# Optimization experiments

Hardware: AMD Instinct MI355X
Metric: run time of the kernel (lower is better)

Reference implementation:

```python
import jax, jax.numpy as jnp
import numpy as np

B = 262144      # points per batch
DIM = 3         # input_dim
L = 16          # levels
T = 19          # log2 hash table size
F = 2           # features per level
N_MIN, N_MAX = 16, 512

_b = np.exp((np.log(N_MAX) - np.log(N_MIN)) / (L - 1))
RES = np.floor(N_MIN * _b ** np.arange(L)).astype(np.float32).reshape(1, 1, L, 1)

# voxel corner offsets [1, DIM, 1, 2^DIM]
_border = np.empty((DIM, 2 ** DIM), dtype=np.uint32)
for i in range(DIM):
    _border[i, :] = np.array(([0] * 2 ** i + [1] * 2 ** i) * 2 ** (DIM - i - 1), dtype=np.uint32)
BORDER = _border.reshape(1, DIM, 1, 2 ** DIM)

# tiny-cuda-nn hash primes; all fit in uint32. Since the torch code takes the
# result mod 2^T (a power of two), int64 and uint32 arithmetic agree on the
# low bits, so uint32 hashing is bit-exact with the original.
PRIMES = np.array([1, 2654435761, 805459861], dtype=np.uint32)
MASK = np.uint32(2 ** T - 1)


def setup_inputs() -> dict:
    key = jax.random.key(0)
    k1, k2 = jax.random.split(key)
    x = jax.random.uniform(k1, (B, DIM), dtype=jnp.float32)  # coords in [0,1)
    tables = jax.random.uniform(k2, (L, 2 ** T, F), dtype=jnp.float32,
                                minval=-1e-4, maxval=1e-4)
    return {"x": x, "tables": tables}


def reference(x, tables):
    res = jnp.asarray(RES)                                   # [1,1,L,1]
    border = jnp.asarray(BORDER)                             # [1,DIM,1,2^DIM]
    primes = jnp.asarray(PRIMES)
    scaled = x[:, :, None, None] * res                       # [B,DIM,L,1]
    grid = jnp.floor(scaled).astype(jnp.uint32) + border     # [B,DIM,L,2^DIM]
    # spatial hash: xor of per-dim coord * prime, mod 2^T
    h = (grid[:, 0] * primes[0]) ^ (grid[:, 1] * primes[1]) ^ (grid[:, 2] * primes[2])
    idx = (h & MASK).astype(jnp.int32)                       # [B,L,2^DIM]
    gathered = tables[jnp.arange(L)[None, :, None], idx]     # [B,L,2^DIM,F]
    # multilinear interpolation weights
    w = jnp.prod(1.0 - jnp.abs(scaled - grid.astype(scaled.dtype)), axis=1)  # [B,L,2^DIM]
    out = jnp.einsum('blv,blvf->blf', w, gathered)           # [B,L,F]
    return out.reshape(x.shape[0], L * F)
```

## Files before the change

### kernel.cpp

```cpp
#include <hip/hip_runtime.h>


#define NB 262144
#define NL 16
#define TSIZE (1u << 19)
#define TMASK ((1u << 19) - 1u)
#define P1 2654435761u
#define P2 805459861u
#define NBKT 32768

typedef float vf2 __attribute__((ext_vector_type(2)));
typedef float vf4 __attribute__((ext_vector_type(4)));

__constant__ float RES_C[NL] = {16.f, 20.f, 25.f, 32.f, 40.f, 50.f, 64.f, 80.f,
                                101.f, 128.f, 161.f, 203.f, 256.f, 322.f, 406.f, 512.f};

__constant__ int SEQ_C[NL] = {0, 15, 1, 14, 2, 13, 3, 12, 4, 11, 5, 10, 6, 9, 7, 8};

__device__ __forceinline__ int bucket_of(float px, float py, float pz) {
  int bx = min(31, (int)(px * 32.0f));
  int by = min(31, (int)(py * 32.0f));
  int bz = min(31, (int)(pz * 32.0f));
  return bx | (by << 5) | (bz << 10);
}

__device__ __forceinline__ void ngp_point_level(
    float px, float py, float pz, int l, const float* __restrict__ tables,
    float& o0, float& o1) {
  const float res = RES_C[l];
  const float sx = px * res, sy = py * res, sz = pz * res;
  const float fx = floorf(sx), fy = floorf(sy), fz = floorf(sz);
  const unsigned ix = (unsigned)fx, iy = (unsigned)fy, iz = (unsigned)fz;

  const unsigned hx0 = ix, hx1 = ix + 1u;
  const unsigned hy0 = iy * P1, hy1 = hy0 + P1;
  const unsigned hz0 = iz * P2, hz1 = hz0 + P2;

  const float wx0 = 1.0f - fabsf(sx - fx);
  const float wx1 = 1.0f - fabsf(sx - (fx + 1.0f));
  const float wy0 = 1.0f - fabsf(sy - fy);
  const float wy1 = 1.0f - fabsf(sy - (fy + 1.0f));
  const float wz0 = 1.0f - fabsf(sz - fz);
  const float wz1 = 1.0f - fabsf(sz - (fz + 1.0f));

  const vf2* __restrict__ tbl = (const vf2*)tables + (size_t)l * TSIZE;

  unsigned idxs[8];
#pragma unroll
  for (int v = 0; v < 8; ++v) {
    const unsigned hx = (v & 1) ? hx1 : hx0;
    const unsigned hy = (v & 2) ? hy1 : hy0;
    const unsigned hz = (v & 4) ? hz1 : hz0;
    idxs[v] = (hx ^ hy ^ hz) & TMASK;
  }
  vf2 g[8];
#pragma unroll
  for (int v = 0; v < 8; ++v) g[v] = tbl[idxs[v]];

  o0 = 0.0f; o1 = 0.0f;
#pragma unroll
  for (int v = 0; v < 8; ++v) {
    const float w = ((v & 1) ? wx1 : wx0) * ((v & 2) ? wy1 : wy0) * ((v & 4) ? wz1 : wz0);
    o0 = fmaf(w, g[v].x, o0);
    o1 = fmaf(w, g[v].y, o1);
  }
}

__global__ __launch_bounds__(256) void zero_kernel(unsigned* __restrict__ hist) {
  hist[blockIdx.x * 256 + threadIdx.x] = 0u;
}

__global__ __launch_bounds__(256) void hist_kernel(
    const float* __restrict__ x, unsigned* __restrict__ hist) {
  const int b = blockIdx.x * 256 + threadIdx.x;
  const float px = x[b * 3 + 0], py = x[b * 3 + 1], pz = x[b * 3 + 2];
  atomicAdd(&hist[bucket_of(px, py, pz)], 1u);
}

__global__ __launch_bounds__(1024) void scan_kernel(
    const unsigned* __restrict__ hist, unsigned* __restrict__ offs) {
  __shared__ unsigned part[1024];
  const int t = threadIdx.x;
  const int base = t * 32;
  unsigned loc[32];
  unsigned s = 0;
#pragma unroll
  for (int i = 0; i < 32; ++i) { loc[i] = s; s += hist[base + i]; }
  part[t] = s;
  __syncthreads();
  for (int d = 1; d < 1024; d <<= 1) {
    unsigned v = (t >= d) ? part[t - d] : 0u;
    __syncthreads();
    part[t] += v;
    __syncthreads();
  }
  const unsigned pre = (t == 0) ? 0u : part[t - 1];
#pragma unroll
  for (int i = 0; i < 32; ++i) offs[base + i] = pre + loc[i];
}

__global__ __launch_bounds__(256) void scatter_kernel(
    const float* __restrict__ x, unsigned* __restrict__ offs,
    vf4* __restrict__ xp) {
  const int b = blockIdx.x * 256 + threadIdx.x;
  const float px = x[b * 3 + 0], py = x[b * 3 + 1], pz = x[b * 3 + 2];
  const unsigned pos = atomicAdd(&offs[bucket_of(px, py, pz)], 1u);
  vf4 v; v.x = px; v.y = py; v.z = pz; v.w = __uint_as_float((unsigned)b);
  xp[pos] = v;
}

__global__ __launch_bounds__(256) void ngp_gather_sorted_kernel(
    const vf4* __restrict__ xp,
    const float* __restrict__ tables,
    vf2* __restrict__ ws) {
  const int i = blockIdx.x;
  const int lvl = SEQ_C[i >> 10];
  const int chunk = i & 1023;
  const int p = chunk * 256 + threadIdx.x;

  const vf4 v = __builtin_nontemporal_load(xp + p);

  float o0, o1;
  ngp_point_level(v.x, v.y, v.z, lvl, tables, o0, o1);

  vf2 r; r.x = o0; r.y = o1;
  __builtin_nontemporal_store(r, ws + (size_t)lvl * NB + p);
}

__global__ __launch_bounds__(256) void ngp_transpose_sorted_kernel(
    const vf2* __restrict__ ws,
    const vf4* __restrict__ xp,
    vf4* __restrict__ out4) {
  __shared__ vf2 tile[NL][257];
  __shared__ unsigned pid[256];
  const int t = threadIdx.x;
  const int p0 = blockIdx.x * 256;

#pragma unroll
  for (int l = 0; l < NL; ++l) {
    tile[l][t] = __builtin_nontemporal_load(ws + (size_t)l * NB + p0 + t);
  }
  pid[t] = __float_as_uint(xp[p0 + t].w);
  __syncthreads();

#pragma unroll
  for (int k = 0; k < 8; ++k) {
    const int q = k * 256 + t;
    const int pq = q >> 3;
    const int wq = q & 7;
    const vf2 a = tile[2 * wq + 0][pq];
    const vf2 c = tile[2 * wq + 1][pq];
    vf4 v; v.x = a.x; v.y = a.y; v.z = c.x; v.w = c.y;
    out4[(size_t)pid[pq] * 8 + wq] = v;
  }
}

__global__ __launch_bounds__(256) void ngp_gather_kernel(
    const float* __restrict__ x, const float* __restrict__ tables,
    vf2* __restrict__ ws) {
  const int i = blockIdx.x;
  const int lvl = (i & 7) | ((i >> 13) << 3);
  const int chunk = (i >> 3) & 1023;
  const int b = chunk * 256 + threadIdx.x;
  const float px = __builtin_nontemporal_load(x + b * 3 + 0);
  const float py = __builtin_nontemporal_load(x + b * 3 + 1);
  const float pz = __builtin_nontemporal_load(x + b * 3 + 2);
  float o0, o1;
  ngp_point_level(px, py, pz, lvl, tables, o0, o1);
  vf2 r; r.x = o0; r.y = o1;
  __builtin_nontemporal_store(r, ws + (size_t)lvl * NB + b);
}

__global__ __launch_bounds__(256) void ngp_transpose_kernel(
    const vf2* __restrict__ ws, vf4* __restrict__ out4) {
  __shared__ vf2 tile[NL][257];
  const int t = threadIdx.x;
  const int p0 = blockIdx.x * 256;
#pragma unroll
  for (int l = 0; l < NL; ++l) {
    tile[l][t] = __builtin_nontemporal_load(ws + (size_t)l * NB + p0 + t);
  }
  __syncthreads();
#pragma unroll
  for (int k = 0; k < 8; ++k) {
    const int q = k * 256 + t;
    const int pq = q >> 3;
    const int wq = q & 7;
    const vf2 a = tile[2 * wq + 0][pq];
    const vf2 c = tile[2 * wq + 1][pq];
    vf4 v; v.x = a.x; v.y = a.y; v.z = c.x; v.w = c.y;
    __builtin_nontemporal_store(v, out4 + (size_t)p0 * 8 + q);
  }
}

__global__ __launch_bounds__(256) void ngp_fused_kernel(
    const float* __restrict__ x, const float* __restrict__ tables,
    float* __restrict__ out) {
  const int tid = blockIdx.x * blockDim.x + threadIdx.x;
  const int l = tid & (NL - 1);
  const int b = tid >> 4;
  float o0, o1;
  ngp_point_level(x[b * 3], x[b * 3 + 1], x[b * 3 + 2], l, tables, o0, o1);
  float2 r = make_float2(o0, o1);
  ((float2*)out)[tid] = r;
}

extern "C" void kernel_launch(void* const* d_in, const int* in_sizes, int n_in,
                              void* d_out, int out_size, void* d_ws, size_t ws_size,
                              hipStream_t stream) {
  const float* x = (const float*)d_in[0];
  const float* tables = (const float*)d_in[1];
  float* out = (float*)d_out;

  const size_t ws2_b = (size_t)NL * NB * sizeof(vf2);
  const size_t xp_b = (size_t)NB * sizeof(vf4);
  const size_t hist_b = (size_t)NBKT * sizeof(unsigned);
  const size_t sorted_need = ws2_b + xp_b + 2 * hist_b;

  if (ws_size >= sorted_need) {
    char* base = (char*)d_ws;
    vf2* ws2 = (vf2*)base;
    vf4* xp = (vf4*)(base + ws2_b);
    unsigned* hist = (unsigned*)(base + ws2_b + xp_b);
    unsigned* offs = (unsigned*)(base + ws2_b + xp_b + hist_b);

    zero_kernel<<<NBKT / 256, 256, 0, stream>>>(hist);
    hist_kernel<<<NB / 256, 256, 0, stream>>>(x, hist);
    scan_kernel<<<1, 1024, 0, stream>>>(hist, offs);
    scatter_kernel<<<NB / 256, 256, 0, stream>>>(x, offs, xp);
    ngp_gather_sorted_kernel<<<NB * NL / 256, 256, 0, stream>>>(xp, tables, ws2);
    ngp_transpose_sorted_kernel<<<NB / 256, 256, 0, stream>>>(ws2, xp, (vf4*)out);
  } else if (ws_size >= ws2_b) {
    vf2* ws = (vf2*)d_ws;
    ngp_gather_kernel<<<NB * NL / 256, 256, 0, stream>>>(x, tables, ws);
    ngp_transpose_kernel<<<NB / 256, 256, 0, stream>>>(ws, (vf4*)out);
  } else {
    ngp_fused_kernel<<<NB * NL / 256, 256, 0, stream>>>(x, tables, out);
  }
}
```

Measured before the change: 204.7 us.

## Coarsen sort buckets, fuse scan into scatter, gather table pairs as float4

Reduces the spatial sort grid from 32^3 to 16^3 buckets. The separate single-block scan kernel is dropped: every scatter block now recomputes the 4096-entry prefix sum in shared memory and takes ranks from a separate counter array, and the zero kernel becomes a memset. The hash lookup now reads 16-byte aligned pairs of table entries and picks the needed half, aiming for wider loads and fewer launches. The costs are coarser sort locality, a redundant per-block scan, and twice the bytes fetched per corner.

```diff
diff --git a/kernel.cpp b/kernel.cpp
--- a/kernel.cpp
+++ b/kernel.cpp
@@ -7,7 +7,7 @@
 #define TMASK ((1u << 19) - 1u)
 #define P1 2654435761u
 #define P2 805459861u
-#define NBKT 32768
+#define NBKT 4096
 
 typedef float vf2 __attribute__((ext_vector_type(2)));
 typedef float vf4 __attribute__((ext_vector_type(4)));
@@ -18,10 +18,10 @@
 __constant__ int SEQ_C[NL] = {0, 15, 1, 14, 2, 13, 3, 12, 4, 11, 5, 10, 6, 9, 7, 8};
 
 __device__ __forceinline__ int bucket_of(float px, float py, float pz) {
-  int bx = min(31, (int)(px * 32.0f));
-  int by = min(31, (int)(py * 32.0f));
-  int bz = min(31, (int)(pz * 32.0f));
-  return bx | (by << 5) | (bz << 10);
+  int bx = min(15, (int)(px * 16.0f));
+  int by = min(15, (int)(py * 16.0f));
+  int bz = min(15, (int)(pz * 16.0f));
+  return bx | (by << 4) | (bz << 8);
 }
 
 __device__ __forceinline__ void ngp_point_level(
@@ -32,7 +32,6 @@
   const float fx = floorf(sx), fy = floorf(sy), fz = floorf(sz);
   const unsigned ix = (unsigned)fx, iy = (unsigned)fy, iz = (unsigned)fz;
 
-  const unsigned hx0 = ix, hx1 = ix + 1u;
   const unsigned hy0 = iy * P1, hy1 = hy0 + P1;
   const unsigned hz0 = iz * P2, hz1 = hz0 + P2;
 
@@ -43,31 +42,32 @@
   const float wz0 = 1.0f - fabsf(sz - fz);
   const float wz1 = 1.0f - fabsf(sz - (fz + 1.0f));
 
-  const vf2* __restrict__ tbl = (const vf2*)tables + (size_t)l * TSIZE;
-
-  unsigned idxs[8];
-#pragma unroll
-  for (int v = 0; v < 8; ++v) {
-    const unsigned hx = (v & 1) ? hx1 : hx0;
-    const unsigned hy = (v & 2) ? hy1 : hy0;
-    const unsigned hz = (v & 4) ? hz1 : hz0;
-    idxs[v] = (hx ^ hy ^ hz) & TMASK;
-  }
-  vf2 g[8];
-#pragma unroll
-  for (int v = 0; v < 8; ++v) g[v] = tbl[idxs[v]];
+  const vf4* __restrict__ tbl4 = (const vf4*)tables + (size_t)l * (TSIZE / 2);
+
+  unsigned hyz[4];
+  hyz[0] = hy0 ^ hz0;
+  hyz[1] = hy1 ^ hz0;
+  hyz[2] = hy0 ^ hz1;
+  hyz[3] = hy1 ^ hz1;
+  float wyz[4];
+  wyz[0] = wy0 * wz0; wyz[1] = wy1 * wz0; wyz[2] = wy0 * wz1; wyz[3] = wy1 * wz1;
 
   o0 = 0.0f; o1 = 0.0f;
 #pragma unroll
-  for (int v = 0; v < 8; ++v) {
-    const float w = ((v & 1) ? wx1 : wx0) * ((v & 2) ? wy1 : wy0) * ((v & 4) ? wz1 : wz0);
-    o0 = fmaf(w, g[v].x, o0);
-    o1 = fmaf(w, g[v].y, o1);
-  }
-}
-
-__global__ __launch_bounds__(256) void zero_kernel(unsigned* __restrict__ hist) {
-  hist[blockIdx.x * 256 + threadIdx.x] = 0u;
+  for (int p = 0; p < 4; ++p) {
+    const unsigned i0 = (ix ^ hyz[p]) & TMASK;
+    const unsigned i1 = ((ix + 1u) ^ hyz[p]) & TMASK;
+    const vf4 q0 = tbl4[i0 >> 1];
+    const vf4 q1 = tbl4[i1 >> 1];
+    const float g0x = (i0 & 1u) ? q0.z : q0.x;
+    const float g0y = (i0 & 1u) ? q0.w : q0.y;
+    const float g1x = (i1 & 1u) ? q1.z : q1.x;
+    const float g1y = (i1 & 1u) ? q1.w : q1.y;
+    const float w0 = wx0 * wyz[p];
+    const float w1 = wx1 * wyz[p];
+    o0 = fmaf(w1, g1x, fmaf(w0, g0x, o0));
+    o1 = fmaf(w1, g1y, fmaf(w0, g0y, o1));
+  }
 }
 
 __global__ __launch_bounds__(256) void hist_kernel(
@@ -77,18 +77,21 @@
   atomicAdd(&hist[bucket_of(px, py, pz)], 1u);
 }
 
-__global__ __launch_bounds__(1024) void scan_kernel(
-    const unsigned* __restrict__ hist, unsigned* __restrict__ offs) {
-  __shared__ unsigned part[1024];
+__global__ __launch_bounds__(256) void scatter_kernel(
+    const float* __restrict__ x, const unsigned* __restrict__ hist,
+    unsigned* __restrict__ cnt, vf4* __restrict__ xp) {
+  __shared__ unsigned soff[NBKT];
+  __shared__ unsigned part[256];
   const int t = threadIdx.x;
-  const int base = t * 32;
-  unsigned loc[32];
+  const int base = t * (NBKT / 256);
+
+  unsigned loc[NBKT / 256];
   unsigned s = 0;
 #pragma unroll
-  for (int i = 0; i < 32; ++i) { loc[i] = s; s += hist[base + i]; }
+  for (int i = 0; i < NBKT / 256; ++i) { loc[i] = s; s += hist[base + i]; }
   part[t] = s;
   __syncthreads();
-  for (int d = 1; d < 1024; d <<= 1) {
+  for (int d = 1; d < 256; d <<= 1) {
     unsigned v = (t >= d) ? part[t - d] : 0u;
     __syncthreads();
     part[t] += v;
@@ -96,15 +99,14 @@
   }
   const unsigned pre = (t == 0) ? 0u : part[t - 1];
 #pragma unroll
-  for (int i = 0; i < 32; ++i) offs[base + i] = pre + loc[i];
-}
-
-__global__ __launch_bounds__(256) void scatter_kernel(
-    const float* __restrict__ x, unsigned* __restrict__ offs,
-    vf4* __restrict__ xp) {
-  const int b = blockIdx.x * 256 + threadIdx.x;
+  for (int i = 0; i < NBKT / 256; ++i) soff[base + i] = pre + loc[i];
+  __syncthreads();
+
+  const int b = blockIdx.x * 256 + t;
   const float px = x[b * 3 + 0], py = x[b * 3 + 1], pz = x[b * 3 + 2];
-  const unsigned pos = atomicAdd(&offs[bucket_of(px, py, pz)], 1u);
+  const int bkt = bucket_of(px, py, pz);
+  const unsigned rank = atomicAdd(&cnt[bkt], 1u);
+  const unsigned pos = soff[bkt] + rank;
   vf4 v; v.x = px; v.y = py; v.z = pz; v.w = __uint_as_float((unsigned)b);
   xp[pos] = v;
 }
@@ -222,12 +224,11 @@
     vf2* ws2 = (vf2*)base;
     vf4* xp = (vf4*)(base + ws2_b);
     unsigned* hist = (unsigned*)(base + ws2_b + xp_b);
-    unsigned* offs = (unsigned*)(base + ws2_b + xp_b + hist_b);
-
-    zero_kernel<<<NBKT / 256, 256, 0, stream>>>(hist);
+    unsigned* cnt = (unsigned*)(base + ws2_b + xp_b + hist_b);
+
+    hipMemsetAsync(hist, 0, 2 * hist_b, stream);
     hist_kernel<<<NB / 256, 256, 0, stream>>>(x, hist);
-    scan_kernel<<<1, 1024, 0, stream>>>(hist, offs);
-    scatter_kernel<<<NB / 256, 256, 0, stream>>>(x, offs, xp);
+    scatter_kernel<<<NB / 256, 256, 0, stream>>>(x, hist, cnt, xp);
     ngp_gather_sorted_kernel<<<NB * NL / 256, 256, 0, stream>>>(xp, tables, ws2);
     ngp_transpose_sorted_kernel<<<NB / 256, 256, 0, stream>>>(ws2, xp, (vf4*)out);
   } else if (ws_size >= ws2_b) {
```

New measurement: 228.5 us. 11.6% more time.
